# Optimization experiments

Hardware: AMD Instinct MI355X
Metric: run time of the kernel (lower is better)

The kernel has to match this reference:

```python
import jax, jax.numpy as jnp
import numpy as np

B, T, C = 4, 1024, 1024
NH, L, DHR, FF = 16, 512, 64, 4096
DK = C // NH  # 64
EPS = 1e-6
NEG = -9e15


def rms_norm(x, w):
    var = jnp.mean(jnp.square(x), axis=-1, keepdims=True)
    return x * jax.lax.rsqrt(var + EPS) * w


def rope_apply(x):
    # Faithful to RoPE module: freq = t+1, pos pairs repeated, theta = exp(-2*pos/C*ln(1e4))
    b, t, c = x.shape
    xf = x.astype(jnp.float32)
    freq = jnp.arange(t, dtype=jnp.float32)[:, None] + 1.0           # [t,1]
    pos = jnp.arange(c // 2, dtype=jnp.float32)[:, None]
    pos = jnp.repeat(pos, 2, axis=-1).reshape(1, -1)                 # [1,c] -> p0,p0,p1,p1,...
    theta = jnp.exp(-2.0 * pos / c * jnp.log(10000.0))
    cos = jnp.cos(freq * theta)                                      # [t,c]
    sin = jnp.sin(freq * theta)
    x2 = xf.reshape(b, t, c // 2, 2)
    rot = jnp.stack([-x2[..., 1], x2[..., 0]], axis=-1).reshape(b, t, c)
    return (xf * cos + rot * sin).astype(x.dtype)


def setup_inputs() -> dict:
    key = jax.random.key(0)
    ks = jax.random.split(key, 12)
    s = 0.02
    return {
        "x": jax.random.normal(ks[0], (B, T, C), jnp.float32),
        "rms1": jnp.ones((C,), jnp.float32),
        "rms2": jnp.ones((C,), jnp.float32),
        "W_dkv": s * jax.random.normal(ks[1], (C, 2 * L), jnp.float32),
        "b_dkv": jnp.zeros((2 * L,), jnp.float32),
        "W_kr": s * jax.random.normal(ks[2], (2 * L, DHR), jnp.float32),
        "b_kr": jnp.zeros((DHR,), jnp.float32),
        "W_qr": s * jax.random.normal(ks[3], (2 * L, DHR * NH), jnp.float32),
        "b_qr": jnp.zeros((DHR * NH,), jnp.float32),
        "W_kv": s * jax.random.normal(ks[4], (L, 2 * C), jnp.float32),
        "b_kv": jnp.zeros((2 * C,), jnp.float32),
        "W_q": s * jax.random.normal(ks[5], (L, C), jnp.float32),
        "b_q": jnp.zeros((C,), jnp.float32),
        "W_o": s * jax.random.normal(ks[6], (C, C), jnp.float32),
        "b_o": jnp.zeros((C,), jnp.float32),
        "W_f1": s * jax.random.normal(ks[7], (C, FF), jnp.float32),
        "b_f1": jnp.zeros((FF,), jnp.float32),
        "W_f2": s * jax.random.normal(ks[8], (FF, C), jnp.float32),
        "b_f2": jnp.zeros((C,), jnp.float32),
    }


def mla(x, W_dkv, b_dkv, W_kr, b_kr, W_qr, b_qr, W_kv, b_kv, W_q, b_q, W_o, b_o):
    b, t, c = x.shape
    comp = jnp.einsum('btc,cd->btd', x, W_dkv) + b_dkv               # [B,T,2L]
    cKV, cq = jnp.split(comp, 2, axis=-1)                            # [B,T,L] each
    # RoPE branches (computed from the compressed representation, as in source)
    kR = rope_apply(jnp.einsum('btl,ld->btd', comp, W_kr) + b_kr)    # [B,T,DHR]
    qR = rope_apply(jnp.einsum('btl,ld->btd', comp, W_qr) + b_qr)    # roped over full NH*DHR dim
    qR = qR.reshape(b, t, NH, DHR).transpose(0, 2, 1, 3)             # [B,NH,T,DHR]
    kv = jnp.einsum('btl,ld->btd', cKV, W_kv) + b_kv
    k, v = jnp.split(kv, 2, axis=-1)                                 # [B,T,C] each
    q = jnp.einsum('btl,ld->btd', cq, W_q) + b_q                     # [B,T,C]
    to_heads = lambda z: z.reshape(b, t, NH, DK).transpose(0, 2, 1, 3)
    q, k, v = to_heads(q), to_heads(k), to_heads(v)                  # [B,NH,T,DK]
    q = jnp.concatenate([q, qR], axis=-1)                            # [B,NH,T,DK+DHR]
    k = jnp.concatenate([k, jnp.broadcast_to(kR[:, None], (b, NH, t, DHR))], axis=-1)
    # manual masked softmax in fp32, scale uses DK (not DK+DHR), faithful to source
    scale = 1.0 / np.sqrt(DK)
    w = jnp.einsum('bnqd,bnkd->bnqk', q.astype(jnp.float32), k.astype(jnp.float32)) * scale
    mask = jnp.tril(jnp.ones((t, t), jnp.float32))
    w = jnp.where(mask == 0, NEG, w)
    p = jax.nn.softmax(w, axis=-1)
    o = jnp.einsum('bnqk,bnkd->bnqd', p, v.astype(jnp.float32)).astype(x.dtype)
    o = o.transpose(0, 2, 1, 3).reshape(b, t, c)
    return jnp.einsum('btc,cd->btd', o, W_o) + b_o


def ffn(x, W_f1, b_f1, W_f2, b_f2):
    h = jax.nn.gelu(jnp.einsum('btc,cf->btf', x, W_f1) + b_f1)
    return jnp.einsum('btf,fc->btc', h, W_f2) + b_f2


def reference(x, rms1, rms2, W_dkv, b_dkv, W_kr, b_kr, W_qr, b_qr,
              W_kv, b_kv, W_q, b_q, W_o, b_o, W_f1, b_f1, W_f2, b_f2):
    h = x + mla(rms_norm(x, rms1), W_dkv, b_dkv, W_kr, b_kr, W_qr, b_qr,
                W_kv, b_kv, W_q, b_q, W_o, b_o)
    out = h + ffn(rms_norm(h, rms2), W_f1, b_f1, W_f2, b_f2)
    return out
```

## Files before the change

kernel.cpp:

```cpp
#include <hip/hip_runtime.h>

typedef unsigned int u32;
typedef unsigned short u16;
typedef __bf16 bf16x8 __attribute__((ext_vector_type(8)));
typedef float f32x4 __attribute__((ext_vector_type(4)));

#define B_ 4
#define T_ 1024
#define C_ 1024
#define NH_ 16
#define L_ 512
#define DHR_ 64
#define FF_ 4096

typedef __attribute__((address_space(3))) u32 as3_u32;
typedef __attribute__((address_space(1))) u32 as1_u32;

__device__ __forceinline__ void gld16(const u16* g, u16* l) {
  __builtin_amdgcn_global_load_lds((const as1_u32*)g, (as3_u32*)l, 16, 0, 0);
}

__device__ __forceinline__ float bf2f(u16 u) {
  union { u32 i; float f; } v; v.i = ((u32)u) << 16; return v.f;
}
__device__ __forceinline__ u16 f2bf(float f) {
  union { float f; u32 i; } v; v.f = f;
  u32 r = (v.i + 0x7FFFu + ((v.i >> 16) & 1u)) >> 16;
  return (u16)r;
}

struct TransArgs {
  const float* src[8];
  u16* dst[8];
  int R[8], C[8];
  int base[9];
  const float* x;
  const float* rmsw;
  u16* xn;
};

__global__ void pre_all(TransArgs ta) {
  const int bid = blockIdx.x;
  if (bid >= ta.base[8]) {
    const int row = bid - ta.base[8];
    const int tid = threadIdx.y * 32 + threadIdx.x;
    const float* xp = ta.x + (size_t)row * C_;
    float v[4];
#pragma unroll
    for (int i = 0; i < 4; i++) v[i] = xp[tid + 256 * i];
    float ss = v[0] * v[0] + v[1] * v[1] + v[2] * v[2] + v[3] * v[3];
#pragma unroll
    for (int o = 32; o > 0; o >>= 1) ss += __shfl_down(ss, o, 64);
    __shared__ float red[4];
    if ((tid & 63) == 0) red[tid >> 6] = ss;
    __syncthreads();
    ss = red[0] + red[1] + red[2] + red[3];
    float scale = rsqrtf(ss * (1.0f / 1024.0f) + 1e-6f);
    u16* op = ta.xn + (size_t)row * C_;
#pragma unroll
    for (int i = 0; i < 4; i++)
      op[tid + 256 * i] = f2bf(v[i] * scale * ta.rmsw[tid + 256 * i]);
    return;
  }
  __shared__ float tile[32][33];
  int w = 0;
#pragma unroll
  for (int i = 1; i < 8; i++) w += (bid >= ta.base[i]);
  const int local = bid - ta.base[w];
  const int R = ta.R[w], C = ta.C[w];
  const int ctiles = C >> 5;
  const int bx = (local % ctiles) * 32;
  const int by = (local / ctiles) * 32;
  const float* in = ta.src[w];
  u16* outp = ta.dst[w];
  const int tx = threadIdx.x, ty = threadIdx.y;
  for (int i = ty; i < 32; i += 8)
    tile[i][tx] = in[(size_t)(by + i) * C + bx + tx];
  __syncthreads();
  for (int i = ty; i < 32; i += 8)
    outp[(size_t)(bx + i) * R + by + tx] = f2bf(tile[tx][i]);
}

__global__ __launch_bounds__(256) void rmsnorm_kernel(const float* __restrict__ xin,
                                                      const float* __restrict__ w,
                                                      u16* __restrict__ outp) {
  const int row = blockIdx.x;
  const int tid = threadIdx.x;
  const float* xp = xin + (size_t)row * C_;
  float v[4];
#pragma unroll
  for (int i = 0; i < 4; i++) v[i] = xp[tid + 256 * i];
  float ss = v[0] * v[0] + v[1] * v[1] + v[2] * v[2] + v[3] * v[3];
#pragma unroll
  for (int o = 32; o > 0; o >>= 1) ss += __shfl_down(ss, o, 64);
  __shared__ float red[4];
  if ((tid & 63) == 0) red[tid >> 6] = ss;
  __syncthreads();
  ss = red[0] + red[1] + red[2] + red[3];
  float scale = rsqrtf(ss * (1.0f / 1024.0f) + 1e-6f);
  u16* op = outp + (size_t)row * C_;
#pragma unroll
  for (int i = 0; i < 4; i++)
    op[tid + 256 * i] = f2bf(v[i] * scale * w[tid + 256 * i]);
}

template<int EPI, bool NCLIP, int NT>
__device__ __forceinline__ void g_body(
    u16* As, u16* Bs,
    const u16* __restrict__ A, int lda, int aoff,
    const u16* __restrict__ BT, const float* __restrict__ bias,
    const float* __restrict__ resid, void* __restrict__ out,
    int N, int Kfull, int Klen, int m0, int n0, int koff) {
  const int tid = threadIdx.x;
  const int wave = tid >> 6, lane = tid & 63;
  const int wm = wave >> 1, wn = wave & 1;
  const int quad = lane >> 4, l15 = lane & 15;
  const int srow = tid >> 3;
  const int gseg = (tid & 7) ^ (srow & 7);

  const u16* aP = A + (size_t)(m0 + srow) * lda + aoff + koff + gseg * 8;
  const u16* bP = BT + (size_t)(n0 + srow) * Kfull + koff + gseg * 8;
  u16* aL = As + tid * 8;
  u16* bL = Bs + tid * 8;
  const size_t aStep = (size_t)32 * lda;
  const size_t bStep = (size_t)32 * Kfull;

  f32x4 acc[4][NT] = {};

  for (int k0 = 0; k0 < Klen; k0 += 64) {
#pragma unroll
    for (int c = 0; c < 4; c++)
      gld16(aP + k0 + c * aStep, aL + c * 32 * 64);
#pragma unroll
    for (int c = 0; c < NT; c++)
      gld16(bP + k0 + c * bStep, bL + c * 32 * 64);
    __syncthreads();
#pragma unroll
    for (int kh = 0; kh < 2; kh++) {
      bf16x8 af[4], bfr[NT];
#pragma unroll
      for (int mt = 0; mt < 4; mt++) {
        const int r = wm * 64 + mt * 16 + l15;
        const int p = (kh * 4 + quad) ^ (r & 7);
        af[mt] = *(const bf16x8*)&As[r * 64 + p * 8];
      }
#pragma unroll
      for (int nt = 0; nt < NT; nt++) {
        const int r = wn * (NT * 16) + nt * 16 + l15;
        const int p = (kh * 4 + quad) ^ (r & 7);
        bfr[nt] = *(const bf16x8*)&Bs[r * 64 + p * 8];
      }
#pragma unroll
      for (int mt = 0; mt < 4; mt++)
#pragma unroll
        for (int nt = 0; nt < NT; nt++)
          acc[mt][nt] = __builtin_amdgcn_mfma_f32_16x16x32_bf16(af[mt], bfr[nt], acc[mt][nt], 0, 0, 0);
    }
    __syncthreads();
  }

  float bvv[NT];
#pragma unroll
  for (int nt = 0; nt < NT; nt++) {
    const int gn = n0 + wn * (NT * 16) + nt * 16 + l15;
    bvv[nt] = (EPI == 4) ? 0.0f : ((NCLIP && gn >= N) ? 0.0f : bias[gn]);
  }
#pragma unroll
  for (int mt = 0; mt < 4; mt++) {
#pragma unroll
    for (int i = 0; i < 4; i++) {
      const int gm = m0 + wm * 64 + mt * 16 + quad * 4 + i;
      const size_t rowb = (size_t)gm * N;
#pragma unroll
      for (int nt = 0; nt < NT; nt++) {
        const int gn = n0 + wn * (NT * 16) + nt * 16 + l15;
        if (NCLIP && gn >= N) continue;
        const size_t oidx = rowb + gn;
        float v = acc[mt][nt][i] + bvv[nt];
        if (EPI == 2) {
          float y = 0.7978845608028654f * (v + 0.044715f * v * v * v);
          float t = __expf(fminf(2.0f * y, 80.0f));
          v = v * t / (t + 1.0f);
        }
        if (EPI == 3) v += resid[oidx];
        if (EPI == 1 || EPI == 3 || EPI == 4) ((float*)out)[oidx] = v;
        else ((u16*)out)[oidx] = f2bf(v);
      }
    }
  }
}

template<int EPI, int NT>
__global__ __launch_bounds__(256) void gemmN(
    const u16* __restrict__ A, int lda, int aoff,
    const u16* __restrict__ BT, const float* __restrict__ bias,
    const float* __restrict__ resid, void* __restrict__ out,
    int N, int K) {
  __shared__ __align__(16) u16 As[128 * 64];
  __shared__ __align__(16) u16 Bs[NT * 32 * 64];
  g_body<EPI, false, NT>(As, Bs, A, lda, aoff, BT, bias, resid, out,
                         N, K, K, blockIdx.x * 128, blockIdx.y * (NT * 32), 0);
}

__global__ __launch_bounds__(256) void gemm128_splitk(
    const u16* __restrict__ A, int lda, const u16* __restrict__ BT,
    float* __restrict__ part, int N, int Kfull, int Klen) {
  __shared__ __align__(16) u16 As[128 * 64];
  __shared__ __align__(16) u16 Bs[128 * 64];
  const int z = blockIdx.z;
  g_body<4, false, 4>(As, Bs, A, lda, 0, BT, nullptr, nullptr,
                      part + (size_t)z * 4096 * N,
                      N, Kfull, Klen, blockIdx.x * 128, blockIdx.y * 128, z * Klen);
}

__global__ __launch_bounds__(256) void f2_reduce(
    const float* __restrict__ part, const float* __restrict__ h,
    const float* __restrict__ bias, float* __restrict__ out) {
  const size_t base = (size_t)blockIdx.x * 1024;
  const size_t PS = (size_t)4096 * 1024;
#pragma unroll
  for (int i = 0; i < 4; i++) {
    const int col = threadIdx.x + 256 * i;
    out[base + col] = h[base + col] + bias[col] + part[base + col] +
                      part[PS + base + col];
  }
}

__global__ __launch_bounds__(256) void proj_fused(
    const u16* __restrict__ comp,
    const u16* __restrict__ WT_qr, const float* __restrict__ b_qr, float* __restrict__ qr_pre,
    const u16* __restrict__ WT_kr, const float* __restrict__ b_kr, float* __restrict__ kr_pre,
    const u16* __restrict__ WT_kv, const float* __restrict__ b_kv, u16* __restrict__ kvbuf,
    const u16* __restrict__ WT_q, const float* __restrict__ b_q, u16* __restrict__ qbuf) {
  __shared__ __align__(16) u16 As[128 * 64];
  __shared__ __align__(16) u16 Bs[128 * 64];
  const int m0 = blockIdx.x * 128;
  const int ny = blockIdx.y;
  if (ny < 8)
    g_body<1, false, 4>(As, Bs, comp, 1024, 0, WT_qr, b_qr, nullptr, qr_pre, 1024, 1024, 1024, m0, ny * 128, 0);
  else if (ny == 8)
    g_body<1, true, 4>(As, Bs, comp, 1024, 0, WT_kr, b_kr, nullptr, kr_pre, 64, 1024, 1024, m0, 0, 0);
  else if (ny < 25)
    g_body<0, false, 4>(As, Bs, comp, 1024, 0, WT_kv, b_kv, nullptr, kvbuf, 2048, 512, 512, m0, (ny - 9) * 128, 0);
  else
    g_body<0, false, 4>(As, Bs, comp, 1024, 512, WT_q, b_q, nullptr, qbuf, 1024, 512, 512, m0, (ny - 25) * 128, 0);
}

__global__ __launch_bounds__(256) void rope_vtrans(
    const u16* __restrict__ qb, const float* __restrict__ qr_pre,
    const u16* __restrict__ kvb, const float* __restrict__ kr_pre,
    u16* __restrict__ Qf, u16* __restrict__ Kf, u16* __restrict__ Vf) {
  __shared__ u16 tile[64][72];
  if (blockIdx.x >= 4096) {
    const int bid2 = blockIdx.x - 4096;
    const int bh = bid2 & 63, t0 = (bid2 >> 6) * 64;
    const int b = bh >> 4, h = bh & 15;
    const int r = threadIdx.x >> 2, seg = (threadIdx.x & 3) * 16;
    const u16* src = &kvb[((size_t)(b * 1024) + t0 + r) * 2048 + 1024 + h * 64 + seg];
    *(uint4*)&tile[r][seg] = *(const uint4*)src;
    *(uint4*)&tile[r][seg + 8] = *(const uint4*)(src + 8);
    __syncthreads();
    const int d = threadIdx.x >> 2, ts = (threadIdx.x & 3) * 16;
    u16 tmp[16];
#pragma unroll
    for (int j = 0; j < 16; j++) tmp[j] = tile[ts + j][d];
    u16* dst = &Vf[((size_t)bh * 64 + d) * 1024 + t0 + ts];
    *(uint4*)dst = *(uint4*)tmp;
    *(uint4*)(dst + 8) = *(uint4*)(tmp + 8);
    return;
  }
  const int bt = blockIdx.x;
  const int b = bt >> 10, t = bt & 1023;
  const float freq = (float)(t + 1);
  for (int idx = threadIdx.x; idx < 2048; idx += 256) {
    const int h = idx >> 7, d = idx & 127;
    const size_t dst = (((size_t)(b * 16 + h)) * T_ + t) * 128 + d;
    u16 qv, kvv;
    if (d < 64) {
      qv = qb[(size_t)bt * C_ + h * 64 + d];
      kvv = kvb[(size_t)bt * 2048 + h * 64 + d];
    } else {
      const int dd = d - 64;
      {
        const int g = h * 64 + dd;
        const int p = g >> 1;
        const float theta = __expf(-(float)(2 * p) * (9.210340372f / 1024.0f));
        float s, c;
        sincosf(freq * theta, &s, &c);
        const float x0 = qr_pre[(size_t)bt * 1024 + (p << 1)];
        const float x1 = qr_pre[(size_t)bt * 1024 + (p << 1) + 1];
        qv = f2bf((g & 1) ? (x1 * c + x0 * s) : (x0 * c - x1 * s));
      }
      {
        const int p = dd >> 1;
        const float theta = __expf(-(float)(2 * p) * (9.210340372f / 64.0f));
        float s, c;
        sincosf(freq * theta, &s, &c);
        const float x0 = kr_pre[(size_t)bt * 64 + (p << 1)];
        const float x1 = kr_pre[(size_t)bt * 64 + (p << 1) + 1];
        kvv = f2bf((dd & 1) ? (x1 * c + x0 * s) : (x0 * c - x1 * s));
      }
    }
    Qf[dst] = qv;
    Kf[dst] = kvv;
  }
}

#define KSTR 136
#define VSTR 72

__device__ __forceinline__ void attn_tile(
    u16* Ks, u16* Vt, u16* Ps,
    const u16* __restrict__ Qf, const u16* __restrict__ Kf,
    const u16* __restrict__ Vf, u16* __restrict__ attn_o,
    int b, int h, int qt) {
  const int tid = threadIdx.x;
  const int wave = tid >> 6, lane = tid & 63;
  const int quad = lane >> 4, l15 = lane & 15;
  const int q0 = qt * 64;
  const size_t bh = (size_t)(b * 16 + h);

  bf16x8 qfrag[4];
  {
    const u16* qb = &Qf[(bh * T_ + q0 + wave * 16 + l15) * 128 + quad * 8];
#pragma unroll
    for (int kc = 0; kc < 4; kc++) qfrag[kc] = *(const bf16x8*)(qb + kc * 32);
  }

  f32x4 acc_o[4] = {};
  float m_i[4], l_i[4];
#pragma unroll
  for (int i = 0; i < 4; i++) { m_i[i] = -3.0e38f; l_i[i] = 0.0f; }

  const int kr_ = tid >> 3, kcs = (tid & 7) * 16;
  const int vd = tid >> 2, vts = (tid & 3) * 16;
  u16* Pw = Ps + wave * 16 * VSTR;

  for (int kt = 0; kt <= qt; kt++) {
    __syncthreads();
    {
      const u16* s0 = &Kf[(bh * T_ + kt * 64 + kr_) * 128 + kcs];
      const u16* s1 = s0 + 32 * 128;
      *(uint4*)&Ks[kr_ * KSTR + kcs] = *(const uint4*)s0;
      *(uint4*)&Ks[kr_ * KSTR + kcs + 8] = *(const uint4*)(s0 + 8);
      *(uint4*)&Ks[(kr_ + 32) * KSTR + kcs] = *(const uint4*)s1;
      *(uint4*)&Ks[(kr_ + 32) * KSTR + kcs + 8] = *(const uint4*)(s1 + 8);
      const u16* vs = &Vf[(bh * 64 + vd) * 1024 + kt * 64 + vts];
      *(uint4*)&Vt[vd * VSTR + vts] = *(const uint4*)vs;
      *(uint4*)&Vt[vd * VSTR + vts + 8] = *(const uint4*)(vs + 8);
    }
    __syncthreads();

    f32x4 acc_s[4] = {};
#pragma unroll
    for (int kc = 0; kc < 4; kc++) {
#pragma unroll
      for (int ng = 0; ng < 4; ng++) {
        bf16x8 bb = *(const bf16x8*)&Ks[(ng * 16 + l15) * KSTR + kc * 32 + quad * 8];
        acc_s[ng] = __builtin_amdgcn_mfma_f32_16x16x32_bf16(qfrag[kc], bb, acc_s[ng], 0, 0, 0);
      }
    }

    float sv[4][4];
#pragma unroll
    for (int ng = 0; ng < 4; ng++)
#pragma unroll
      for (int i = 0; i < 4; i++) {
        float s = acc_s[ng][i] * 0.125f;
        if (kt == qt && (ng * 16 + l15) > (wave * 16 + quad * 4 + i)) s = -3.0e38f;
        sv[ng][i] = s;
      }

    float alpha[4], mx[4];
#pragma unroll
    for (int i = 0; i < 4; i++) {
      float m = fmaxf(fmaxf(sv[0][i], sv[1][i]), fmaxf(sv[2][i], sv[3][i]));
#pragma unroll
      for (int off = 1; off < 16; off <<= 1) m = fmaxf(m, __shfl_xor(m, off, 64));
      float mn = fmaxf(m_i[i], m);
      alpha[i] = __expf(m_i[i] - mn);
      m_i[i] = mn;
      mx[i] = mn;
    }
    float rs[4] = {0.f, 0.f, 0.f, 0.f};
#pragma unroll
    for (int ng = 0; ng < 4; ng++)
#pragma unroll
      for (int i = 0; i < 4; i++) {
        float p = __expf(sv[ng][i] - mx[i]);
        rs[i] += p;
        Pw[(quad * 4 + i) * VSTR + ng * 16 + l15] = f2bf(p);
      }
#pragma unroll
    for (int i = 0; i < 4; i++) {
      float r = rs[i];
#pragma unroll
      for (int off = 1; off < 16; off <<= 1) r += __shfl_xor(r, off, 64);
      l_i[i] = l_i[i] * alpha[i] + r;
    }

#pragma unroll
    for (int ng = 0; ng < 4; ng++)
#pragma unroll
      for (int i = 0; i < 4; i++) acc_o[ng][i] *= alpha[i];
#pragma unroll
    for (int kc = 0; kc < 2; kc++) {
      bf16x8 a = *(const bf16x8*)&Pw[l15 * VSTR + kc * 32 + quad * 8];
#pragma unroll
      for (int ng = 0; ng < 4; ng++) {
        bf16x8 bb = *(const bf16x8*)&Vt[(ng * 16 + l15) * VSTR + kc * 32 + quad * 8];
        acc_o[ng] = __builtin_amdgcn_mfma_f32_16x16x32_bf16(a, bb, acc_o[ng], 0, 0, 0);
      }
    }
  }

  float linv[4];
#pragma unroll
  for (int i = 0; i < 4; i++) linv[i] = 1.0f / l_i[i];
#pragma unroll
  for (int ng = 0; ng < 4; ng++)
#pragma unroll
    for (int i = 0; i < 4; i++) {
      const int qrow = q0 + wave * 16 + quad * 4 + i;
      attn_o[((size_t)(b * T_) + qrow) * C_ + h * 64 + ng * 16 + l15] =
          f2bf(acc_o[ng][i] * linv[i]);
    }
}

__global__ __launch_bounds__(256) void attn_mfma(
    const u16* __restrict__ Qf, const u16* __restrict__ Kf,
    const u16* __restrict__ Vf, u16* __restrict__ attn_o) {
  __shared__ __align__(16) u16 Ks[64 * KSTR];
  __shared__ __align__(16) u16 Vt[64 * VSTR];
  __shared__ __align__(16) u16 Ps[4 * 16 * VSTR];
  const int j = blockIdx.x & 7;
  const int h = (blockIdx.x >> 3) & 15;
  const int b = blockIdx.x >> 7;
  attn_tile(Ks, Vt, Ps, Qf, Kf, Vf, attn_o, b, h, 15 - j);
  attn_tile(Ks, Vt, Ps, Qf, Kf, Vf, attn_o, b, h, j);
}

extern "C" void kernel_launch(void* const* d_in, const int* in_sizes, int n_in,
                              void* d_out, int out_size, void* d_ws, size_t ws_size,
                              hipStream_t stream) {
  const float* x = (const float*)d_in[0];
  const float* rms1 = (const float*)d_in[1];
  const float* rms2 = (const float*)d_in[2];
  const float* W_dkv = (const float*)d_in[3];
  const float* b_dkv = (const float*)d_in[4];
  const float* W_kr = (const float*)d_in[5];
  const float* b_kr = (const float*)d_in[6];
  const float* W_qr = (const float*)d_in[7];
  const float* b_qr = (const float*)d_in[8];
  const float* W_kv = (const float*)d_in[9];
  const float* b_kv = (const float*)d_in[10];
  const float* W_q = (const float*)d_in[11];
  const float* b_q = (const float*)d_in[12];
  const float* W_o = (const float*)d_in[13];
  const float* b_o = (const float*)d_in[14];
  const float* W_f1 = (const float*)d_in[15];
  const float* b_f1 = (const float*)d_in[16];
  const float* W_f2 = (const float*)d_in[17];
  const float* b_f2 = (const float*)d_in[18];
  float* out = (float*)d_out;

  char* ws = (char*)d_ws;
  size_t off = 0;
  auto alloc = [&](size_t bytes) -> void* {
    void* p = ws + off;
    off += (bytes + 255) & ~(size_t)255;
    return p;
  };
  u16* WT_dkv = (u16*)alloc((size_t)1024 * 1024 * 2);
  u16* WT_kr  = (u16*)alloc((size_t)128 * 1024 * 2);
  u16* WT_qr  = (u16*)alloc((size_t)1024 * 1024 * 2);
  u16* WT_kv  = (u16*)alloc((size_t)2048 * 512 * 2);
  u16* WT_q   = (u16*)alloc((size_t)1024 * 512 * 2);
  u16* WT_o   = (u16*)alloc((size_t)1024 * 1024 * 2);
  u16* WT_f1  = (u16*)alloc((size_t)4096 * 1024 * 2);
  u16* WT_f2  = (u16*)alloc((size_t)1024 * 4096 * 2);
  u16* xn1    = (u16*)alloc((size_t)4096 * 1024 * 2);
  u16* comp   = (u16*)alloc((size_t)4096 * 1024 * 2);
  float* kr_pre = (float*)alloc((size_t)4096 * 64 * 4);
  float* qr_pre = (float*)alloc((size_t)4096 * 1024 * 4);
  u16* kvbuf  = (u16*)alloc((size_t)4096 * 2048 * 2);
  u16* qbuf   = (u16*)alloc((size_t)4096 * 1024 * 2);
  u16* Qf     = (u16*)alloc((size_t)64 * 1024 * 128 * 2);
  u16* Kf     = (u16*)alloc((size_t)64 * 1024 * 128 * 2);
  u16* Vf     = (u16*)alloc((size_t)64 * 64 * 1024 * 2);
  u16* attn_o = (u16*)alloc((size_t)4096 * 1024 * 2);
  float* hbuf = (float*)alloc((size_t)4096 * 1024 * 4);
  u16* hn     = (u16*)alloc((size_t)4096 * 1024 * 2);
  u16* hid    = (u16*)alloc((size_t)4096 * 4096 * 2);
  float* partial = (float*)Qf;

  TransArgs ta;
  const float* srcs[8] = {W_dkv, W_kr, W_qr, W_kv, W_q, W_o, W_f1, W_f2};
  u16* dsts[8] = {WT_dkv, WT_kr, WT_qr, WT_kv, WT_q, WT_o, WT_f1, WT_f2};
  const int Rs[8] = {1024, 1024, 1024, 512, 512, 1024, 1024, 4096};
  const int Cs[8] = {1024, 64, 1024, 2048, 1024, 1024, 4096, 1024};
  int acc_t = 0;
  for (int i = 0; i < 8; i++) {
    ta.src[i] = srcs[i]; ta.dst[i] = dsts[i]; ta.R[i] = Rs[i]; ta.C[i] = Cs[i];
    ta.base[i] = acc_t;
    acc_t += (Rs[i] >> 5) * (Cs[i] >> 5);
  }
  ta.base[8] = acc_t;
  ta.x = x; ta.rmsw = rms1; ta.xn = xn1;
  pre_all<<<acc_t + 4096, dim3(32, 8), 0, stream>>>(ta);

  gemmN<0, 2><<<dim3(32, 16), 256, 0, stream>>>(xn1, 1024, 0, WT_dkv, b_dkv, nullptr, comp, 1024, 1024);

  proj_fused<<<dim3(32, 33), 256, 0, stream>>>(comp,
      WT_qr, b_qr, qr_pre, WT_kr, b_kr, kr_pre,
      WT_kv, b_kv, kvbuf, WT_q, b_q, qbuf);

  rope_vtrans<<<4096 + 1024, 256, 0, stream>>>(qbuf, qr_pre, kvbuf, kr_pre, Qf, Kf, Vf);

  attn_mfma<<<B_ * NH_ * 8, 256, 0, stream>>>(Qf, Kf, Vf, attn_o);

  gemmN<3, 2><<<dim3(32, 16), 256, 0, stream>>>(attn_o, 1024, 0, WT_o, b_o, x, hbuf, 1024, 1024);

  rmsnorm_kernel<<<4096, 256, 0, stream>>>(hbuf, rms2, hn);

  gemmN<2, 4><<<dim3(32, 32), 256, 0, stream>>>(hn, 1024, 0, WT_f1, b_f1, nullptr, hid, 4096, 1024);

  gemm128_splitk<<<dim3(32, 8, 2), 256, 0, stream>>>(hid, 4096, WT_f2, partial, 1024, 4096, 2048);
  f2_reduce<<<4096, 256, 0, stream>>>(partial, hbuf, b_f2, out);
}
```

Before: 421.2 us.

## Read K directly from kvbuf and shared rope kR instead of materializing per-head Kf

The rope kernel no longer builds a full per-head K tensor (B*NH*T*128). It writes only a small shared rotated kR buffer, computed once per token by the h==0 lanes. The attention kernel now loads the K part straight from kvbuf and the rope part from kRf, which removes about 16 MB of writes and the repeated kR sincos work. Attention block indexing also changes so that blocks for different heads with the same query-tile pair are adjacent, which may change cache locality and scheduling order.

```diff
diff --git a/kernel.cpp b/kernel.cpp
--- a/kernel.cpp
+++ b/kernel.cpp
@@ -249,7 +249,7 @@
 __global__ __launch_bounds__(256) void rope_vtrans(
     const u16* __restrict__ qb, const float* __restrict__ qr_pre,
     const u16* __restrict__ kvb, const float* __restrict__ kr_pre,
-    u16* __restrict__ Qf, u16* __restrict__ Kf, u16* __restrict__ Vf) {
+    u16* __restrict__ Qf, u16* __restrict__ kRf, u16* __restrict__ Vf) {
   __shared__ u16 tile[64][72];
   if (blockIdx.x >= 4096) {
     const int bid2 = blockIdx.x - 4096;
@@ -275,34 +275,28 @@
   for (int idx = threadIdx.x; idx < 2048; idx += 256) {
     const int h = idx >> 7, d = idx & 127;
     const size_t dst = (((size_t)(b * 16 + h)) * T_ + t) * 128 + d;
-    u16 qv, kvv;
     if (d < 64) {
-      qv = qb[(size_t)bt * C_ + h * 64 + d];
-      kvv = kvb[(size_t)bt * 2048 + h * 64 + d];
+      Qf[dst] = qb[(size_t)bt * C_ + h * 64 + d];
     } else {
       const int dd = d - 64;
-      {
-        const int g = h * 64 + dd;
-        const int p = g >> 1;
-        const float theta = __expf(-(float)(2 * p) * (9.210340372f / 1024.0f));
-        float s, c;
-        sincosf(freq * theta, &s, &c);
-        const float x0 = qr_pre[(size_t)bt * 1024 + (p << 1)];
-        const float x1 = qr_pre[(size_t)bt * 1024 + (p << 1) + 1];
-        qv = f2bf((g & 1) ? (x1 * c + x0 * s) : (x0 * c - x1 * s));
-      }
-      {
-        const int p = dd >> 1;
-        const float theta = __expf(-(float)(2 * p) * (9.210340372f / 64.0f));
-        float s, c;
-        sincosf(freq * theta, &s, &c);
-        const float x0 = kr_pre[(size_t)bt * 64 + (p << 1)];
-        const float x1 = kr_pre[(size_t)bt * 64 + (p << 1) + 1];
-        kvv = f2bf((dd & 1) ? (x1 * c + x0 * s) : (x0 * c - x1 * s));
-      }
-    }
-    Qf[dst] = qv;
-    Kf[dst] = kvv;
+      const int g = h * 64 + dd;
+      const int p = g >> 1;
+      const float theta = __expf(-(float)(2 * p) * (9.210340372f / 1024.0f));
+      float s, c;
+      sincosf(freq * theta, &s, &c);
+      const float x0 = qr_pre[(size_t)bt * 1024 + (p << 1)];
+      const float x1 = qr_pre[(size_t)bt * 1024 + (p << 1) + 1];
+      Qf[dst] = f2bf((g & 1) ? (x1 * c + x0 * s) : (x0 * c - x1 * s));
+      if (h == 0) {
+        const int p2 = dd >> 1;
+        const float theta2 = __expf(-(float)(2 * p2) * (9.210340372f / 64.0f));
+        float s2, c2;
+        sincosf(freq * theta2, &s2, &c2);
+        const float y0 = kr_pre[(size_t)bt * 64 + (p2 << 1)];
+        const float y1 = kr_pre[(size_t)bt * 64 + (p2 << 1) + 1];
+        kRf[(size_t)bt * 64 + dd] = f2bf((dd & 1) ? (y1 * c2 + y0 * s2) : (y0 * c2 - y1 * s2));
+      }
+    }
   }
 }
 
@@ -311,9 +305,9 @@
 
 __device__ __forceinline__ void attn_tile(
     u16* Ks, u16* Vt, u16* Ps,
-    const u16* __restrict__ Qf, const u16* __restrict__ Kf,
-    const u16* __restrict__ Vf, u16* __restrict__ attn_o,
-    int b, int h, int qt) {
+    const u16* __restrict__ Qf, const u16* __restrict__ kvbuf,
+    const u16* __restrict__ kRf, const u16* __restrict__ Vf,
+    u16* __restrict__ attn_o, int b, int h, int qt) {
   const int tid = threadIdx.x;
   const int wave = tid >> 6, lane = tid & 63;
   const int quad = lane >> 4, l15 = lane & 15;
@@ -336,11 +330,17 @@
   const int vd = tid >> 2, vts = (tid & 3) * 16;
   u16* Pw = Ps + wave * 16 * VSTR;
 
+  const bool isk = kcs < 64;
+  const size_t rstep = isk ? (size_t)32 * 2048 : (size_t)32 * 64;
+
   for (int kt = 0; kt <= qt; kt++) {
     __syncthreads();
     {
-      const u16* s0 = &Kf[(bh * T_ + kt * 64 + kr_) * 128 + kcs];
-      const u16* s1 = s0 + 32 * 128;
+      const int t_row = kt * 64 + kr_;
+      const u16* s0 = isk
+          ? &kvbuf[((size_t)(b * T_) + t_row) * 2048 + h * 64 + kcs]
+          : &kRf[((size_t)(b * T_) + t_row) * 64 + (kcs - 64)];
+      const u16* s1 = s0 + rstep;
       *(uint4*)&Ks[kr_ * KSTR + kcs] = *(const uint4*)s0;
       *(uint4*)&Ks[kr_ * KSTR + kcs + 8] = *(const uint4*)(s0 + 8);
       *(uint4*)&Ks[(kr_ + 32) * KSTR + kcs] = *(const uint4*)s1;
@@ -428,16 +428,18 @@
 }
 
 __global__ __launch_bounds__(256) void attn_mfma(
-    const u16* __restrict__ Qf, const u16* __restrict__ Kf,
-    const u16* __restrict__ Vf, u16* __restrict__ attn_o) {
+    const u16* __restrict__ Qf, const u16* __restrict__ kvbuf,
+    const u16* __restrict__ kRf, const u16* __restrict__ Vf,
+    u16* __restrict__ attn_o) {
   __shared__ __align__(16) u16 Ks[64 * KSTR];
   __shared__ __align__(16) u16 Vt[64 * VSTR];
   __shared__ __align__(16) u16 Ps[4 * 16 * VSTR];
-  const int j = blockIdx.x & 7;
-  const int h = (blockIdx.x >> 3) & 15;
-  const int b = blockIdx.x >> 7;
-  attn_tile(Ks, Vt, Ps, Qf, Kf, Vf, attn_o, b, h, 15 - j);
-  attn_tile(Ks, Vt, Ps, Qf, Kf, Vf, attn_o, b, h, j);
+  const int bh_lin = blockIdx.x & 63;
+  const int j = blockIdx.x >> 6;
+  const int h = bh_lin & 15;
+  const int b = bh_lin >> 4;
+  attn_tile(Ks, Vt, Ps, Qf, kvbuf, kRf, Vf, attn_o, b, h, 15 - j);
+  attn_tile(Ks, Vt, Ps, Qf, kvbuf, kRf, Vf, attn_o, b, h, j);
 }
 
 extern "C" void kernel_launch(void* const* d_in, const int* in_sizes, int n_in,
@@ -486,7 +488,7 @@
   u16* kvbuf  = (u16*)alloc((size_t)4096 * 2048 * 2);
   u16* qbuf   = (u16*)alloc((size_t)4096 * 1024 * 2);
   u16* Qf     = (u16*)alloc((size_t)64 * 1024 * 128 * 2);
-  u16* Kf     = (u16*)alloc((size_t)64 * 1024 * 128 * 2);
+  u16* kRf    = (u16*)alloc((size_t)4096 * 64 * 2);
   u16* Vf     = (u16*)alloc((size_t)64 * 64 * 1024 * 2);
   u16* attn_o = (u16*)alloc((size_t)4096 * 1024 * 2);
   float* hbuf = (float*)alloc((size_t)4096 * 1024 * 4);
@@ -515,9 +517,9 @@
       WT_qr, b_qr, qr_pre, WT_kr, b_kr, kr_pre,
       WT_kv, b_kv, kvbuf, WT_q, b_q, qbuf);
 
-  rope_vtrans<<<4096 + 1024, 256, 0, stream>>>(qbuf, qr_pre, kvbuf, kr_pre, Qf, Kf, Vf);
-
-  attn_mfma<<<B_ * NH_ * 8, 256, 0, stream>>>(Qf, Kf, Vf, attn_o);
+  rope_vtrans<<<4096 + 1024, 256, 0, stream>>>(qbuf, qr_pre, kvbuf, kr_pre, Qf, kRf, Vf);
+
+  attn_mfma<<<B_ * NH_ * 8, 256, 0, stream>>>(Qf, kvbuf, kRf, Vf, attn_o);
 
   gemmN<3, 2><<<dim3(32, 16), 256, 0, stream>>>(attn_o, 1024, 0, WT_o, b_o, x, hbuf, 1024, 1024);
 
```

Measured after the change: 416.5 us. Within noise of the previous version (-1.1%).
